# Performance work log

Hardware: AMD Instinct MI355X
Metric: run time of the kernel (lower is better)

## Reference

```python
import jax, jax.numpy as jnp
import numpy as np
import math

HIDDEN = 1024

def setup_inputs() -> dict:
    key = jax.random.key(0)
    k1, k2, k3, k4, k5 = jax.random.split(key, 5)
    s = 1.0 / math.sqrt(HIDDEN)
    return {
        "x": jax.random.normal(k1, (4, 2048, HIDDEN), dtype=jnp.float32),
        "W_qkv": jax.random.uniform(k2, (HIDDEN, 3 * HIDDEN), jnp.float32, -s, s),
        "b_qkv": jax.random.uniform(k3, (3 * HIDDEN,), jnp.float32, -s, s),
        "W_out": jax.random.uniform(k4, (HIDDEN, HIDDEN), jnp.float32, -s, s),
        "b_out": jax.random.uniform(k5, (HIDDEN,), jnp.float32, -s, s),
    }

def reference(x, W_qkv, b_qkv, W_out, b_out):
    # fused QKV projection: [b, s, 3h]
    qkv = jnp.einsum("bsh,hd->bsd", x, W_qkv) + b_qkv
    q, k, v = jnp.split(qkv, 3, axis=-1)
    scale = 1.0 / math.sqrt(x.shape[-1])
    scores = jnp.einsum("bqh,bkh->bqk", q, k) * scale  # [b, s, s]
    attn = jax.nn.softmax(scores, axis=-1)
    out = jnp.einsum("bqk,bkh->bqh", attn, v)
    return jnp.einsum("bsh,hd->bsd", out, W_out) + b_out
```

## Files before the change

kernel.cpp:

```cpp
#include <hip/hip_runtime.h>
#include <cstdint>
#include <cstddef>


typedef __bf16 bf16;
typedef __bf16 bf16x8 __attribute__((ext_vector_type(8)));
typedef __bf16 bf16x4 __attribute__((ext_vector_type(4)));
typedef float  f32x4  __attribute__((ext_vector_type(4)));

#define UNIT 8192
#define U97  4096

__device__ __forceinline__ void gload_lds16(const bf16* g, bf16* l) {
  __builtin_amdgcn_global_load_lds(
      (const __attribute__((address_space(1))) unsigned int*)g,
      (__attribute__((address_space(3))) unsigned int*)l, 16, 0, 0);
}

#define GATE(N)  asm volatile("s_waitcnt vmcnt(" #N ")" ::: "memory")
#define LGKM0()  asm volatile("s_waitcnt lgkmcnt(0)" ::: "memory")
#define SBAR()   __builtin_amdgcn_s_barrier()
#define SCHED0() __builtin_amdgcn_sched_barrier(0)

__device__ __forceinline__ void stage97(const bf16* g0, long ld, bf16* u, int tid) {
  const int wv = tid >> 6;
  #pragma unroll
  for (int j = 0; j < 2; ++j) {
    const int c = j * 256 + tid;
    const int r = c >> 2, s = c & 3;
    const int sg = s ^ ((r >> 1) & 3);
    const int cb = j * 256 + (wv << 6);
    gload_lds16(g0 + (long)r * ld + sg * 8, u + (size_t)cb * 8);
  }
}

__device__ __forceinline__ bf16x8 rd97(const bf16* u, int r, int s) {
  return *(const bf16x8*)(u + (size_t)r * 32 + (size_t)((s ^ ((r >> 1) & 3)) * 8));
}

template <int MODE>
__device__ __forceinline__ void gemm97_body(
    const bf16* __restrict__ A, long sAz, int lda,
    const bf16* __restrict__ B, long sBz, int ldb, int K,
    bf16* __restrict__ p0, long sCz, int ldc,
    bf16* __restrict__ p1, bf16* __restrict__ p2,
    float* __restrict__ fout, long sFz,
    const float* __restrict__ bias, const float* __restrict__ Spart, float scale) {
  __shared__ bf16 lds[3][3][U97];
  __shared__ float rinvs[128];
  const int tid = threadIdx.x;
  const int wv = tid >> 6, ln = tid & 63;
  const int wr = wv >> 1, wc = wv & 1;
  const int lr = ln & 15, lh = ln >> 4;
  const int m0 = blockIdx.x * 128, n0 = blockIdx.y * 256;
  const int z = blockIdx.z;
  const bf16* Ag = A + (long)z * sAz + (long)m0 * lda;
  const bf16* Bg = B + (long)z * sBz + (long)n0 * ldb;
  const int NT = K / 32;

  #pragma unroll
  for (int t = 0; t < 2; ++t) {
    stage97(Ag + t * 32,              lda, &lds[t][0][0], tid);
    stage97(Bg + t * 32,              ldb, &lds[t][1][0], tid);
    stage97(Bg + 128 * ldb + t * 32,  ldb, &lds[t][2][0], tid);
  }
  if constexpr (MODE == 3) {
    if (tid < 128) {
      const float* p = Spart + ((size_t)z * 8) * 2048 + m0 + tid;
      float s = 0.f;
      #pragma unroll
      for (int b = 0; b < 8; ++b) s += p[(size_t)b * 2048];
      rinvs[tid] = 1.0f / s;
    }
    LGKM0();
  }
  GATE(6);
  SBAR();
  SCHED0();

  f32x4 acc[4][8];
  #pragma unroll
  for (int i = 0; i < 4; ++i)
    #pragma unroll
    for (int j = 0; j < 8; ++j) acc[i][j] = f32x4{0.f, 0.f, 0.f, 0.f};

  int rs = 0, ns = 2;
  for (int t = 0; t < NT; ++t) {
    const bool pf = (t + 2 < NT);
    bf16x8 aF[4], bF[8];
    #pragma unroll
    for (int i = 0; i < 4; ++i)
      aF[i] = rd97(&lds[rs][0][0], wr * 64 + i * 16 + lr, lh);
    #pragma unroll
    for (int j = 0; j < 8; ++j)
      bF[j] = rd97(&lds[rs][1 + wc][0], j * 16 + lr, lh);
    if (pf) {
      stage97(Ag + (long)(t + 2) * 32,             lda, &lds[ns][0][0], tid);
      stage97(Bg + (long)(t + 2) * 32,             ldb, &lds[ns][1][0], tid);
      stage97(Bg + 128 * ldb + (long)(t + 2) * 32, ldb, &lds[ns][2][0], tid);
    }
    __builtin_amdgcn_s_setprio(1);
    #pragma unroll
    for (int i = 0; i < 4; ++i)
      #pragma unroll
      for (int j = 0; j < 8; ++j)
        acc[i][j] = __builtin_amdgcn_mfma_f32_16x16x32_bf16(aF[i], bF[j], acc[i][j], 0, 0, 0);
    __builtin_amdgcn_s_setprio(0);
    if (t + 1 < NT) {
      if (pf) { GATE(6); } else { GATE(0); }
      SBAR();
      SCHED0();
    }
    rs = (rs == 2) ? 0 : rs + 1;
    ns = (ns == 2) ? 0 : ns + 1;
  }

  #pragma unroll
  for (int mf = 0; mf < 4; ++mf) {
    #pragma unroll
    for (int nf = 0; nf < 8; ++nf) {
      #pragma unroll
      for (int rg = 0; rg < 4; ++rg) {
        const int gm = m0 + wr * 64 + mf * 16 + lh * 4 + rg;
        const int gn = n0 + wc * 128 + nf * 16 + lr;
        float v = acc[mf][nf][rg];
        if constexpr (MODE == 0) {
          v += bias[gn];
          if (gn < 1024)       p0[(size_t)gm * 1024 + gn] = (bf16)v;
          else if (gn < 2048)  p1[(size_t)gm * 1024 + (gn - 1024)] = (bf16)v;
          else                 p2[(size_t)gm * 1024 + (gn - 2048)] = (bf16)v;
        } else if constexpr (MODE == 2) {
          p0[(size_t)z * sCz + (size_t)gm * ldc + gn] = (bf16)(v * scale);
        } else {
          fout[(size_t)z * sFz + (size_t)gm * ldc + gn] =
              v * rinvs[gm - m0] + bias[gn];
        }
      }
    }
  }
}

#define G97_ARGS const bf16* A, long sAz, int lda, const bf16* B, long sBz, int ldb, \
                 int K, bf16* p0, long sCz, int ldc, bf16* p1, bf16* p2,             \
                 float* fout, long sFz, const float* bias, const float* Spart, float scale
__global__ __launch_bounds__(256, 2) void gemm_qkv(G97_ARGS) {
  gemm97_body<0>(A, sAz, lda, B, sBz, ldb, K, p0, sCz, ldc, p1, p2, fout, sFz, bias, Spart, scale);
}
__global__ __launch_bounds__(256, 2) void gemm_vwt(G97_ARGS) {
  gemm97_body<2>(A, sAz, lda, B, sBz, ldb, K, p0, sCz, ldc, p1, p2, fout, sFz, bias, Spart, scale);
}
__global__ __launch_bounds__(256, 2) void gemm_pvw(G97_ARGS) {
  gemm97_body<3>(A, sAz, lda, B, sBz, ldb, K, p0, sCz, ldc, p1, p2, fout, sFz, bias, Spart, scale);
}

#define THREADS8 512

__device__ __forceinline__ void stage_unit(const bf16* g0, long ld, bf16* ldsu, int tid) {
  const int wv = tid >> 6;
  #pragma unroll
  for (int j = 0; j < 2; ++j) {
    const int c = j * 512 + tid;
    const int r = c >> 3;
    const int sg = (c & 7) ^ (r & 7);
    const int cb = j * 512 + (wv << 6);
    gload_lds16(g0 + (long)r * ld + sg * 8, ldsu + (size_t)cb * 8);
  }
}

__device__ __forceinline__ bf16x8 rd_frag(const bf16* unitb, int r, int s) {
  return *(const bf16x8*)(unitb + (size_t)r * 64 + (size_t)((s ^ (r & 7)) * 8));
}

#define PHASE(DB, MH, NH, RA, RB, STAGE_CODE, GATE_CODE)                         \
  {                                                                              \
    if (RA) {                                                                    \
      _Pragma("unroll") for (int mf = 0; mf < 4; ++mf)                           \
        _Pragma("unroll") for (int ks = 0; ks < 2; ++ks)                         \
          aF[mf][ks] = rd_frag(&lds[DB][MH][0], wsm * 64 + mf * 16 + lr, ks * 4 + lh); \
    }                                                                            \
    if (RB) {                                                                    \
      _Pragma("unroll") for (int nf = 0; nf < 2; ++nf)                           \
        _Pragma("unroll") for (int ks = 0; ks < 2; ++ks)                         \
          bF[NH][nf][ks] = rd_frag(&lds[DB][2 + NH][0], wsn * 32 + nf * 16 + lr, ks * 4 + lh); \
    }                                                                            \
    STAGE_CODE;                                                                  \
    SBAR();                                                                      \
    LGKM0();                                                                     \
    SCHED0();                                                                    \
    __builtin_amdgcn_s_setprio(1);                                               \
    _Pragma("unroll") for (int mf = 0; mf < 4; ++mf)                             \
      _Pragma("unroll") for (int nf = 0; nf < 2; ++nf)                           \
        _Pragma("unroll") for (int ks = 0; ks < 2; ++ks)                         \
          acc[(MH)*4 + mf][(NH)*2 + nf] = __builtin_amdgcn_mfma_f32_16x16x32_bf16( \
              aF[mf][ks], bF[NH][nf][ks], acc[(MH)*4 + mf][(NH)*2 + nf], 0, 0, 0); \
    __builtin_amdgcn_s_setprio(0);                                               \
    GATE_CODE;                                                                   \
    SBAR();                                                                      \
    SCHED0();                                                                    \
  }

__global__ __launch_bounds__(THREADS8, 2) void gemm_sc(
    const bf16* __restrict__ A, long sAz, int lda,
    const bf16* __restrict__ B, long sBz, int ldb, int K,
    bf16* __restrict__ p0, long sCz, float* __restrict__ Spart, float scale) {
  __shared__ bf16 lds[2][4][UNIT];
  const int tid = threadIdx.x;
  const int wv = tid >> 6, ln = tid & 63;
  const int wsm = wv >> 2, wsn = wv & 3;
  const int lr = ln & 15, lh = ln >> 4;

  const int gx = gridDim.x, gy = gridDim.y;
  const int lin = blockIdx.x + gx * (blockIdx.y + gy * blockIdx.z);
  const int nwg = gx * gy * gridDim.z;
  const int swz = (lin & 7) * (nwg >> 3) + (lin >> 3);
  const int by = swz % gy;
  const int t2 = swz / gy;
  const int bx = t2 % gx;
  const int z  = t2 / gx;

  const int m0 = bx * 256, n0 = by * 256;
  const bf16* Ag = A + (long)z * sAz + (long)m0 * lda;
  const bf16* Bg = B + (long)z * sBz + (long)n0 * ldb;
  const int NITER = K / 128;

  stage_unit(Ag,             lda, &lds[0][0][0], tid);
  stage_unit(Bg,             ldb, &lds[0][2][0], tid);
  stage_unit(Ag + 128 * lda, lda, &lds[0][1][0], tid);
  stage_unit(Bg + 128 * ldb, ldb, &lds[0][3][0], tid);
  stage_unit(Ag + 64,        lda, &lds[1][0][0], tid);
  stage_unit(Bg + 64,        ldb, &lds[1][2][0], tid);
  GATE(8);
  SBAR();
  SCHED0();

  f32x4 acc[8][4];
  #pragma unroll
  for (int i = 0; i < 8; ++i)
    #pragma unroll
    for (int j = 0; j < 4; ++j) acc[i][j] = f32x4{0.f, 0.f, 0.f, 0.f};
  bf16x8 aF[4][2], bF[2][2][2];

  for (int it = 0; it < NITER; ++it) {
    const bool nl = (it + 1 < NITER);
    const long ktA = 2L * it + 1, ktB = 2L * it + 2, ktC = 2L * it + 3;
    PHASE(0, 0, 0, 1, 1,
      { stage_unit(Ag + 128 * lda + ktA * 64, lda, &lds[1][1][0], tid); },
      { GATE(6); });
    PHASE(0, 0, 1, 0, 1,
      { stage_unit(Bg + 128 * ldb + ktA * 64, ldb, &lds[1][3][0], tid); },
      { GATE(10); });
    PHASE(0, 1, 0, 1, 0,
      { if (nl) stage_unit(Ag + ktB * 64, lda, &lds[0][0][0], tid); },
      {});
    PHASE(0, 1, 1, 0, 0,
      { if (nl) stage_unit(Bg + ktB * 64, ldb, &lds[0][2][0], tid); },
      { if (nl) { GATE(8); } else { GATE(4); } });
    PHASE(1, 0, 0, 1, 1,
      { if (nl) stage_unit(Ag + 128 * lda + ktB * 64, lda, &lds[0][1][0], tid); },
      { if (nl) { GATE(6); } else { GATE(0); } });
    PHASE(1, 0, 1, 0, 1,
      { if (nl) stage_unit(Bg + 128 * ldb + ktB * 64, ldb, &lds[0][3][0], tid); },
      { GATE(10); });
    PHASE(1, 1, 0, 1, 0,
      { if (nl) stage_unit(Ag + ktC * 64, lda, &lds[1][0][0], tid); },
      {});
    PHASE(1, 1, 1, 0, 0,
      { if (nl) stage_unit(Bg + ktC * 64, ldb, &lds[1][2][0], tid); },
      { GATE(8); });
  }

  float ps[8][4];
  #pragma unroll
  for (int mi = 0; mi < 8; ++mi)
    #pragma unroll
    for (int rg = 0; rg < 4; ++rg) ps[mi][rg] = 0.f;

  #pragma unroll
  for (int mi = 0; mi < 8; ++mi) {
    #pragma unroll
    for (int ni = 0; ni < 4; ++ni) {
      #pragma unroll
      for (int rg = 0; rg < 4; ++rg) {
        const int gm = m0 + (mi >> 2) * 128 + wsm * 64 + (mi & 3) * 16 + lh * 4 + rg;
        const int gn = n0 + (ni >> 1) * 128 + wsn * 32 + (ni & 1) * 16 + lr;
        float e = __expf(acc[mi][ni][rg] * scale);
        ps[mi][rg] += e;
        p0[(size_t)z * sCz + (size_t)gm * 2048 + gn] = (bf16)e;
      }
    }
  }
  #pragma unroll
  for (int mi = 0; mi < 8; ++mi) {
    #pragma unroll
    for (int rg = 0; rg < 4; ++rg) {
      float v = ps[mi][rg];
      v += __shfl_xor(v, 1); v += __shfl_xor(v, 2);
      v += __shfl_xor(v, 4); v += __shfl_xor(v, 8);
      ps[mi][rg] = v;
    }
  }
  float* part = (float*)&lds[0][0][0];
  if (lr == 0) {
    #pragma unroll
    for (int mi = 0; mi < 8; ++mi)
      #pragma unroll
      for (int rg = 0; rg < 4; ++rg) {
        const int rl = (mi >> 2) * 128 + wsm * 64 + (mi & 3) * 16 + lh * 4 + rg;
        part[rl * 4 + wsn] = ps[mi][rg];
      }
  }
  __syncthreads();
  if (tid < 256) {
    float s = part[tid * 4] + part[tid * 4 + 1] + part[tid * 4 + 2] + part[tid * 4 + 3];
    Spart[((size_t)(z * 8 + by)) * 2048 + bx * 256 + tid] = s;
  }
}

__global__ __launch_bounds__(256) void k_prep(
    const float* __restrict__ x, bf16* __restrict__ Xb,
    const float* __restrict__ Wqkv, bf16* __restrict__ WqT,
    const float* __restrict__ Wout, bf16* __restrict__ WoT) {
  const int b = blockIdx.x;
  const int tid = threadIdx.x;
  if (b < 4096) {
    long i = ((long)b * 256 + tid) * 8;
    float4 v0 = *(const float4*)(x + i);
    float4 v1 = *(const float4*)(x + i + 4);
    bf16x8 o;
    o[0] = (bf16)v0.x; o[1] = (bf16)v0.y; o[2] = (bf16)v0.z; o[3] = (bf16)v0.w;
    o[4] = (bf16)v1.x; o[5] = (bf16)v1.y; o[6] = (bf16)v1.z; o[7] = (bf16)v1.w;
    *(bf16x8*)(Xb + i) = o;
    return;
  }
  __shared__ float t[32][33];
  const int tx = tid & 31, ty = tid >> 5;
  const float* in;  bf16* out;  int R, C, bx, by;
  if (b < 4096 + 3072) {
    in = Wqkv; out = WqT; R = 1024; C = 3072;
    bx = (b - 4096) % 96; by = (b - 4096) / 96;
  } else {
    in = Wout; out = WoT; R = 1024; C = 1024;
    bx = (b - 7168) % 32; by = (b - 7168) / 32;
  }
  const int c0 = bx * 32, r0 = by * 32;
  #pragma unroll
  for (int dy = 0; dy < 32; dy += 8)
    t[ty + dy][tx] = in[(size_t)(r0 + ty + dy) * C + c0 + tx];
  __syncthreads();
  #pragma unroll
  for (int dy = 0; dy < 32; dy += 8)
    out[(size_t)(c0 + ty + dy) * R + r0 + tx] = (bf16)t[tx][ty + dy];
}

extern "C" void kernel_launch(void* const* d_in, const int* in_sizes, int n_in,
                              void* d_out, int out_size, void* d_ws, size_t ws_size,
                              hipStream_t stream) {
  const float* x    = (const float*)d_in[0];
  const float* Wqkv = (const float*)d_in[1];
  const float* bqkv = (const float*)d_in[2];
  const float* Wout = (const float*)d_in[3];
  const float* bout = (const float*)d_in[4];
  float* out = (float*)d_out;

  char* w = (char*)d_ws;
  const size_t MB = 1ull << 20;
  bf16*  Xb     = (bf16*)(w);
  float* Spart  = (float*)(w);
  bf16* WqT = (bf16*)(w + 16 * MB);
  bf16* WoT = (bf16*)(w + 22 * MB);
  bf16* Qb  = (bf16*)(w + 24 * MB);
  bf16* Kb  = (bf16*)(w + 40 * MB);
  bf16* Vb  = (bf16*)(w + 56 * MB);
  bf16* Sb  = (bf16*)(w + 72 * MB);
  bf16* VWT = (bf16*)(w + 104 * MB);

  k_prep<<<8192, 256, 0, stream>>>(x, Xb, Wqkv, WqT, Wout, WoT);

  gemm_qkv<<<dim3(64, 12), 256, 0, stream>>>(
      Xb, 0L, 1024, WqT, 0L, 1024, 1024,
      Qb, 0L, 1024, Kb, Vb, nullptr, 0L, bqkv, nullptr, 1.0f);

  gemm_vwt<<<dim3(8, 8, 4), 256, 0, stream>>>(
      WoT, 0L, 1024, Vb, 2048L * 1024, 1024, 1024,
      VWT, 1024L * 2048, 2048, nullptr, nullptr, nullptr, 0L, nullptr, nullptr, 1.0f);

  gemm_sc<<<dim3(8, 8, 4), THREADS8, 0, stream>>>(
      Qb, 2048L * 1024, 1024, Kb, 2048L * 1024, 1024, 1024,
      Sb, 2048L * 2048, Spart, 0.03125f);

  gemm_pvw<<<dim3(16, 4, 4), 256, 0, stream>>>(
      Sb, 2048L * 2048, 2048, VWT, 1024L * 2048, 2048, 2048,
      nullptr, 0L, 1024, nullptr, nullptr, out, 2048L * 1024, bout, Spart, 1.0f);
}
```

Before: 200.7 us.

## Deepen GEMM LDS pipeline to six stages with two K-steps per barrier

The shared GEMM body moves from a three-slot LDS ring with one barrier per 32-wide K step to a six-slot ring that prefetches two K steps at a time, four steps ahead, and synchronises once per pair. The aim is to halve the number of barriers and vmcnt waits and to hide more global-load latency. LDS use doubles to about 144 KB per block, and launch bounds drop to one block per CU, which costs occupancy and latency hiding from a second resident block.

Measured after the change: 235.7 us. +17.4%, slower.

```diff
diff --git a/kernel.cpp b/kernel.cpp
--- a/kernel.cpp
+++ b/kernel.cpp
@@ -46,7 +46,7 @@
     bf16* __restrict__ p1, bf16* __restrict__ p2,
     float* __restrict__ fout, long sFz,
     const float* __restrict__ bias, const float* __restrict__ Spart, float scale) {
-  __shared__ bf16 lds[3][3][U97];
+  __shared__ bf16 lds[6][3][U97];
   __shared__ float rinvs[128];
   const int tid = threadIdx.x;
   const int wv = tid >> 6, ln = tid & 63;
@@ -57,12 +57,13 @@
   const bf16* Ag = A + (long)z * sAz + (long)m0 * lda;
   const bf16* Bg = B + (long)z * sBz + (long)n0 * ldb;
   const int NT = K / 32;
-
-  #pragma unroll
-  for (int t = 0; t < 2; ++t) {
-    stage97(Ag + t * 32,              lda, &lds[t][0][0], tid);
-    stage97(Bg + t * 32,              ldb, &lds[t][1][0], tid);
-    stage97(Bg + 128 * ldb + t * 32,  ldb, &lds[t][2][0], tid);
+  const int NW = NT >> 1;
+
+  #pragma unroll
+  for (int t = 0; t < 4; ++t) {
+    stage97(Ag + t * 32,             lda, &lds[t][0][0], tid);
+    stage97(Bg + t * 32,             ldb, &lds[t][1][0], tid);
+    stage97(Bg + 128 * ldb + t * 32, ldb, &lds[t][2][0], tid);
   }
   if constexpr (MODE == 3) {
     if (tid < 128) {
@@ -74,7 +75,7 @@
     }
     LGKM0();
   }
-  GATE(6);
+  GATE(12);
   SBAR();
   SCHED0();
 
@@ -84,35 +85,45 @@
     #pragma unroll
     for (int j = 0; j < 8; ++j) acc[i][j] = f32x4{0.f, 0.f, 0.f, 0.f};
 
-  int rs = 0, ns = 2;
-  for (int t = 0; t < NT; ++t) {
-    const bool pf = (t + 2 < NT);
-    bf16x8 aF[4], bF[8];
-    #pragma unroll
-    for (int i = 0; i < 4; ++i)
-      aF[i] = rd97(&lds[rs][0][0], wr * 64 + i * 16 + lr, lh);
-    #pragma unroll
-    for (int j = 0; j < 8; ++j)
-      bF[j] = rd97(&lds[rs][1 + wc][0], j * 16 + lr, lh);
+  int rsl = 0, ssl = 4;
+  for (int w = 0; w < NW; ++w) {
+    const int t0 = 2 * w;
+    const bool pf = (t0 + 4 < NT);
     if (pf) {
-      stage97(Ag + (long)(t + 2) * 32,             lda, &lds[ns][0][0], tid);
-      stage97(Bg + (long)(t + 2) * 32,             ldb, &lds[ns][1][0], tid);
-      stage97(Bg + 128 * ldb + (long)(t + 2) * 32, ldb, &lds[ns][2][0], tid);
-    }
-    __builtin_amdgcn_s_setprio(1);
-    #pragma unroll
-    for (int i = 0; i < 4; ++i)
+      #pragma unroll
+      for (int q = 0; q < 2; ++q) {
+        const long tt = t0 + 4 + q;
+        bf16* slot = &lds[ssl + q][0][0];
+        stage97(Ag + tt * 32,             lda, slot,            tid);
+        stage97(Bg + tt * 32,             ldb, slot + U97,      tid);
+        stage97(Bg + 128 * ldb + tt * 32, ldb, slot + 2 * U97,  tid);
+      }
+    }
+    #pragma unroll
+    for (int q = 0; q < 2; ++q) {
+      const bf16* slot = &lds[rsl + q][0][0];
+      bf16x8 aF[4], bF[8];
+      #pragma unroll
+      for (int i = 0; i < 4; ++i)
+        aF[i] = rd97(slot, wr * 64 + i * 16 + lr, lh);
       #pragma unroll
       for (int j = 0; j < 8; ++j)
-        acc[i][j] = __builtin_amdgcn_mfma_f32_16x16x32_bf16(aF[i], bF[j], acc[i][j], 0, 0, 0);
-    __builtin_amdgcn_s_setprio(0);
-    if (t + 1 < NT) {
-      if (pf) { GATE(6); } else { GATE(0); }
+        bF[j] = rd97(slot + (1 + wc) * U97, j * 16 + lr, lh);
+      __builtin_amdgcn_s_setprio(1);
+      #pragma unroll
+      for (int i = 0; i < 4; ++i)
+        #pragma unroll
+        for (int j = 0; j < 8; ++j)
+          acc[i][j] = __builtin_amdgcn_mfma_f32_16x16x32_bf16(aF[i], bF[j], acc[i][j], 0, 0, 0);
+      __builtin_amdgcn_s_setprio(0);
+    }
+    if (w + 1 < NW) {
+      if (pf) { GATE(12); } else { GATE(0); }
       SBAR();
       SCHED0();
     }
-    rs = (rs == 2) ? 0 : rs + 1;
-    ns = (ns == 2) ? 0 : ns + 1;
+    rsl = (rsl == 4) ? 0 : rsl + 2;
+    ssl = (ssl == 4) ? 0 : ssl + 2;
   }
 
   #pragma unroll
@@ -143,13 +154,13 @@
 #define G97_ARGS const bf16* A, long sAz, int lda, const bf16* B, long sBz, int ldb, \
                  int K, bf16* p0, long sCz, int ldc, bf16* p1, bf16* p2,             \
                  float* fout, long sFz, const float* bias, const float* Spart, float scale
-__global__ __launch_bounds__(256, 2) void gemm_qkv(G97_ARGS) {
+__global__ __launch_bounds__(256, 1) void gemm_qkv(G97_ARGS) {
   gemm97_body<0>(A, sAz, lda, B, sBz, ldb, K, p0, sCz, ldc, p1, p2, fout, sFz, bias, Spart, scale);
 }
-__global__ __launch_bounds__(256, 2) void gemm_vwt(G97_ARGS) {
+__global__ __launch_bounds__(256, 1) void gemm_vwt(G97_ARGS) {
   gemm97_body<2>(A, sAz, lda, B, sBz, ldb, K, p0, sCz, ldc, p1, p2, fout, sFz, bias, Spart, scale);
 }
-__global__ __launch_bounds__(256, 2) void gemm_pvw(G97_ARGS) {
+__global__ __launch_bounds__(256, 1) void gemm_pvw(G97_ARGS) {
   gemm97_body<3>(A, sAz, lda, B, sBz, ldb, K, p0, sCz, ldc, p1, p2, fout, sFz, bias, Spart, scale);
 }
 
```
